# Performance work log

Measured on AMD Instinct MI355X. Metric: run time of the kernel, lower is better.

## Reference

```python
import jax, jax.numpy as jnp
import numpy as np

HEADS = 4
OUT_DIM = 64
NEG_SLOPE = 0.2


def setup_inputs() -> dict:
    key = jax.random.key(0)
    k1, k2, k3, k4 = jax.random.split(key, 4)
    n, in_dim = 4096, 256
    x = jax.random.normal(k1, (n, in_dim), dtype=jnp.float32)
    adj = jax.random.randint(k2, (n, n), 0, 2, dtype=jnp.int32)
    # lin: in_dim -> heads*out_dim (no bias), stored as [in_dim, heads*out_dim]
    W = jax.random.normal(k3, (in_dim, HEADS * OUT_DIM), dtype=jnp.float32) * 0.05
    # att_weight: [heads, 2*out_dim]
    att = jax.random.normal(k4, (HEADS, 2 * OUT_DIM), dtype=jnp.float32) * 0.05
    return {"x": x, "adj": adj, "W": W, "att": att}


def reference(x, adj, W, att):
    n = x.shape[0]
    h = (x @ W).reshape(n, HEADS, OUT_DIM)  # [n, H, D]
    # scores[i,j,h] = att[h] . cat(h_i, h_j) = <h_i, a_src[h]> + <h_j, a_dst[h]>
    a_src, a_dst = att[:, :OUT_DIM], att[:, OUT_DIM:]
    e_src = jnp.einsum('nhd,hd->nh', h, a_src)  # [n, H]
    e_dst = jnp.einsum('nhd,hd->nh', h, a_dst)  # [n, H]
    scores = e_src[:, None, :] + e_dst[None, :, :]  # [n, n, H]
    scores = jax.nn.leaky_relu(scores, negative_slope=NEG_SLOPE)
    mask = (adj > 0)[:, :, None]  # [n, n, 1]
    scores = jnp.where(mask, scores, -jnp.inf)
    alpha = jax.nn.softmax(scores, axis=1)  # softmax over neighbors j
    # h_prime[i,h,d] = sum_j alpha[i,j,h] * h[j,h,d]
    h_prime = jnp.einsum('ijh,jhd->ihd', alpha, h)
    return h_prime.reshape(n, HEADS * OUT_DIM)
```

## Files before the change

kernel.cpp:

```cpp
#include <hip/hip_runtime.h>
#include <hip/hip_bf16.h>

#define HEADS 4
#define ODIM 64
#define HD 256
#define NEG_SLOPE 0.2f
#define SPLITS 8

typedef __attribute__((ext_vector_type(8))) short bf16x8;
typedef __attribute__((ext_vector_type(4))) float floatx4;
typedef __attribute__((ext_vector_type(2))) float floatx2;

__global__ __launch_bounds__(256) void pack_xw(const float* __restrict__ x,
                                               const float* __restrict__ W,
                                               __hip_bfloat16* __restrict__ xh,
                                               __hip_bfloat16* __restrict__ xl,
                                               __hip_bfloat16* __restrict__ wh,
                                               __hip_bfloat16* __restrict__ wl,
                                               int K, int nxb) {
    const int b = blockIdx.x;
    const int Kc = K >> 5;
    if (b < nxb) {
        const int g = b * 256 + threadIdx.x;
        const int lane = g & 63, frag = g >> 6;
        const int kc = frag % Kc, mc = frag / Kc;
        const int l16 = lane & 15, q = lane >> 4;
        const float* src = x + (size_t)(mc * 16 + l16) * K + kc * 32 + q * 8;
        const float4 v0 = *(const float4*)src;
        const float4 v1 = *(const float4*)(src + 4);
        const float vv[8] = {v0.x, v0.y, v0.z, v0.w, v1.x, v1.y, v1.z, v1.w};
        union { __hip_bfloat16 b[8]; bf16x8 v; } H, L;
        #pragma unroll
        for (int p = 0; p < 8; ++p) {
            H.b[p] = __float2bfloat16(vv[p]);
            L.b[p] = __float2bfloat16(vv[p] - __bfloat162float(H.b[p]));
        }
        *(bf16x8*)&xh[(size_t)frag * 512 + lane * 8] = H.v;
        *(bf16x8*)&xl[(size_t)frag * 512 + lane * 8] = L.v;
    } else {
        const int g = (b - nxb) * 256 + threadIdx.x;
        const int lane = g & 63, frag = g >> 6;
        const int kc = frag % Kc, nc = frag / Kc;
        const int l16 = lane & 15, q = lane >> 4;
        union { __hip_bfloat16 b[8]; bf16x8 v; } H, L;
        #pragma unroll
        for (int p = 0; p < 8; ++p) {
            const float w = W[(size_t)(kc * 32 + q * 8 + p) * HD + nc * 16 + l16];
            H.b[p] = __float2bfloat16(w);
            L.b[p] = __float2bfloat16(w - __bfloat162float(H.b[p]));
        }
        *(bf16x8*)&wh[(size_t)frag * 512 + lane * 8] = H.v;
        *(bf16x8*)&wl[(size_t)frag * 512 + lane * 8] = L.v;
    }
}

__global__ __launch_bounds__(128) void gemm_fused(
    const __hip_bfloat16* __restrict__ xh, const __hip_bfloat16* __restrict__ xl,
    const __hip_bfloat16* __restrict__ wh, const __hip_bfloat16* __restrict__ wl,
    const float* __restrict__ att, float2* __restrict__ esrc, float2* __restrict__ edst,
    __hip_bfloat16* __restrict__ hbB, int n, int K) {

    __shared__ __hip_bfloat16 T[64][40];

    const int tid = threadIdx.x, wave = tid >> 6, lane = tid & 63;
    const int q = lane >> 4, l16 = lane & 15;
    const int m0 = blockIdx.x * 32;
    const int head = blockIdx.y;
    const int Kc = K >> 5;
    const int mc = (m0 >> 4) + wave;

    floatx4 acc[4] = {{0.f,0.f,0.f,0.f},{0.f,0.f,0.f,0.f},{0.f,0.f,0.f,0.f},{0.f,0.f,0.f,0.f}};

    const __hip_bfloat16* Axh = xh + (size_t)mc * Kc * 512 + lane * 8;
    const __hip_bfloat16* Axl = xl + (size_t)mc * Kc * 512 + lane * 8;
    const __hip_bfloat16* Bwh = wh + lane * 8;
    const __hip_bfloat16* Bwl = wl + lane * 8;
    #pragma unroll 2
    for (int kc = 0; kc < Kc; ++kc) {
        const bf16x8 ah = *(const bf16x8*)(Axh + (size_t)kc * 512);
        const bf16x8 al = *(const bf16x8*)(Axl + (size_t)kc * 512);
        bf16x8 bh[4], bl[4];
        #pragma unroll
        for (int nt = 0; nt < 4; ++nt) {
            const size_t fo = (size_t)((head * 4 + nt) * Kc + kc) * 512;
            bh[nt] = *(const bf16x8*)(Bwh + fo);
            bl[nt] = *(const bf16x8*)(Bwl + fo);
        }
        #pragma unroll
        for (int nt = 0; nt < 4; ++nt)
            acc[nt] = __builtin_amdgcn_mfma_f32_16x16x32_bf16(ah, bh[nt], acc[nt], 0, 0, 0);
        #pragma unroll
        for (int nt = 0; nt < 4; ++nt)
            acc[nt] = __builtin_amdgcn_mfma_f32_16x16x32_bf16(ah, bl[nt], acc[nt], 0, 0, 0);
        #pragma unroll
        for (int nt = 0; nt < 4; ++nt)
            acc[nt] = __builtin_amdgcn_mfma_f32_16x16x32_bf16(al, bh[nt], acc[nt], 0, 0, 0);
    }

    float as_v[4], ad_v[4];
    #pragma unroll
    for (int nt = 0; nt < 4; ++nt) {
        as_v[nt] = att[head * 2 * ODIM + nt * 16 + l16];
        ad_v[nt] = att[head * 2 * ODIM + ODIM + nt * 16 + l16];
    }
    #pragma unroll
    for (int r = 0; r < 4; ++r) {
        float ps = 0.f, pd = 0.f;
        #pragma unroll
        for (int nt = 0; nt < 4; ++nt) {
            ps = fmaf(acc[nt][r], as_v[nt], ps);
            pd = fmaf(acc[nt][r], ad_v[nt], pd);
        }
        #pragma unroll
        for (int m = 1; m <= 8; m <<= 1) {
            ps += __shfl_xor(ps, m, 64);
            pd += __shfl_xor(pd, m, 64);
        }
        if (l16 == 0) {
            const int i = m0 + wave * 16 + q * 4 + r;
            esrc[head * n + i] = make_float2(__expf(ps), __expf(NEG_SLOPE * ps));
            edst[head * n + i] = make_float2(__expf(pd), __expf(NEG_SLOPE * pd));
        }
    }

    #pragma unroll
    for (int nt = 0; nt < 4; ++nt) {
        union { __hip_bfloat16 b[4]; uint2 u; } pk;
        #pragma unroll
        for (int r = 0; r < 4; ++r) pk.b[r] = __float2bfloat16(acc[nt][r]);
        *(uint2*)&T[nt * 16 + l16][wave * 16 + q * 4] = pk.u;
    }
    __syncthreads();

    #pragma unroll
    for (int ffi = 0; ffi < 2; ++ffi) {
        const int f = wave + ffi * 2;
        const bf16x8 v = *(const bf16x8*)&T[f * 16 + l16][q * 8];
        const size_t frag = ((size_t)head * (n >> 5) + (m0 >> 5)) * 4 + f;
        *(bf16x8*)&hbB[frag * 512 + lane * 8] = v;
    }
}

__global__ __launch_bounds__(256, 3) void aggregate(
    const int* __restrict__ adj, const float2* __restrict__ esrc,
    const float2* __restrict__ edst, const __hip_bfloat16* __restrict__ hbB,
    float* __restrict__ outsp, float* __restrict__ densp, int n, int KR) {

    __shared__ unsigned char bitsL[32][68];
    __shared__ float2 edL[HEADS][512];

    const int tid = threadIdx.x;
    const int wave = tid >> 6, lane = tid & 63;
    const int q = lane >> 4, l16 = lane & 15;
    const int i0 = blockIdx.x * 32;
    const int K0 = blockIdx.y * KR;

    {
        const int r0 = i0 + wave * 8;
        #pragma unroll
        for (int rr = 0; rr < 8; ++rr) {
            const int4* ap = (const int4*)(adj + (size_t)(r0 + rr) * n + K0 + lane * 8);
            const int4 a = ap[0], b = ap[1];
            unsigned int by = (unsigned int)(a.x > 0)
                            | ((unsigned int)(a.y > 0) << 1)
                            | ((unsigned int)(a.z > 0) << 2)
                            | ((unsigned int)(a.w > 0) << 3)
                            | ((unsigned int)(b.x > 0) << 4)
                            | ((unsigned int)(b.y > 0) << 5)
                            | ((unsigned int)(b.z > 0) << 6)
                            | ((unsigned int)(b.w > 0) << 7);
            bitsL[wave * 8 + rr][lane] = (unsigned char)by;
        }
    }
    for (int t = tid; t < HEADS * 512; t += 256) {
        const int h = t >> 9, j = t & 511;
        edL[h][j] = edst[(size_t)h * n + K0 + j];
    }

    floatx2 es12[2];
    #pragma unroll
    for (int mt = 0; mt < 2; ++mt) {
        const float2 e = esrc[wave * n + i0 + mt * 16 + l16];
        es12[mt][0] = e.x; es12[mt][1] = e.y;
    }

    union { short s[8]; bf16x8 v; } bones;
    #pragma unroll
    for (int p = 0; p < 8; ++p) bones.s[p] = (l16 == 0) ? (short)0x3F80 : (short)0;

    floatx4 acc[2][4];
    floatx4 accd[2];
    #pragma unroll
    for (int mt = 0; mt < 2; ++mt) {
        accd[mt] = (floatx4){0.f, 0.f, 0.f, 0.f};
        #pragma unroll
        for (int nt = 0; nt < 4; ++nt) acc[mt][nt] = (floatx4){0.f, 0.f, 0.f, 0.f};
    }

    __syncthreads();

    const __hip_bfloat16* hb = hbB + ((size_t)wave * (n >> 5) + (K0 >> 5)) * 4 * 512 + lane * 8;
    const int NSTEP = KR >> 5;

    auto loadBF = [&](int s, bf16x8* dst) {
        #pragma unroll
        for (int nt = 0; nt < 4; ++nt)
            dst[nt] = *(const bf16x8*)&hb[((size_t)s * 4 + nt) * 512];
    };

    auto computeStep = [&](int s, const bf16x8* bfr) {
        const unsigned int bm0 = (*(const unsigned int*)&bitsL[l16][s * 4] >> (q * 8)) & 0xFFu;
        const unsigned int bm1 = (*(const unsigned int*)&bitsL[16 + l16][s * 4] >> (q * 8)) & 0xFFu;
        const float4* ep = (const float4*)&edL[wave][s * 32 + q * 8];
        const float4 e01 = ep[0], e23 = ep[1], e45 = ep[2], e67 = ep[3];
        floatx2 ed[8];
        ed[0][0]=e01.x; ed[0][1]=e01.y;  ed[1][0]=e01.z; ed[1][1]=e01.w;
        ed[2][0]=e23.x; ed[2][1]=e23.y;  ed[3][0]=e23.z; ed[3][1]=e23.w;
        ed[4][0]=e45.x; ed[4][1]=e45.y;  ed[5][0]=e45.z; ed[5][1]=e45.w;
        ed[6][0]=e67.x; ed[6][1]=e67.y;  ed[7][0]=e67.z; ed[7][1]=e67.w;
        #pragma unroll
        for (int mt = 0; mt < 2; ++mt) {
            const unsigned int bm = mt ? bm1 : bm0;
            union { unsigned int u[4]; bf16x8 v; } af;
            #pragma unroll
            for (int p = 0; p < 4; ++p) {
                const floatx2 pa = es12[mt] * ed[2 * p];
                const floatx2 pb = es12[mt] * ed[2 * p + 1];
                const float wa = fmaxf(pa[0], pa[1]);
                const float wb = fmaxf(pb[0], pb[1]);
                const unsigned int mm = ((bm >> (2 * p)) & 1u) * 0xFFFFu
                                      | ((bm >> (2 * p + 1)) & 1u) * 0xFFFF0000u;
                af.u[p] = __builtin_amdgcn_perm(__float_as_uint(wb), __float_as_uint(wa),
                                                0x07060302u) & mm;
            }
            #pragma unroll
            for (int nt = 0; nt < 4; ++nt)
                acc[mt][nt] = __builtin_amdgcn_mfma_f32_16x16x32_bf16(af.v, bfr[nt], acc[mt][nt], 0, 0, 0);
            accd[mt] = __builtin_amdgcn_mfma_f32_16x16x32_bf16(af.v, bones.v, accd[mt], 0, 0, 0);
        }
    };

    bf16x8 bA[4], bB[4];
    loadBF(0, bA);
    loadBF(1, bB);
    for (int s = 0; s < NSTEP; s += 2) {
        computeStep(s, bA);
        if (s + 2 < NSTEP) loadBF(s + 2, bA);
        computeStep(s + 1, bB);
        if (s + 3 < NSTEP) loadBF(s + 3, bB);
    }

    const size_t sOut = (size_t)blockIdx.y * n * HD;
    #pragma unroll
    for (int mt = 0; mt < 2; ++mt)
        #pragma unroll
        for (int nt = 0; nt < 4; ++nt)
            #pragma unroll
            for (int r = 0; r < 4; ++r)
                outsp[sOut + (size_t)(i0 + mt * 16 + q * 4 + r) * HD + wave * ODIM + nt * 16 + l16] = acc[mt][nt][r];
    if (l16 == 0) {
        #pragma unroll
        for (int mt = 0; mt < 2; ++mt)
            #pragma unroll
            for (int r = 0; r < 4; ++r)
                densp[((size_t)blockIdx.y * n + i0 + mt * 16 + q * 4 + r) * HEADS + wave] = accd[mt][r];
    }
}

__global__ __launch_bounds__(256) void normalize(const float* __restrict__ outsp,
                                                 const float* __restrict__ densp,
                                                 float* __restrict__ out, int n, int splits) {
    const int g = blockIdx.x * 256 + threadIdx.x;
    const int i = g >> 6;
    const int c4 = (g & 63) * 4;
    const int head = c4 >> 6;
    float den = 0.f;
    for (int s = 0; s < splits; ++s) den += densp[((size_t)s * n + i) * HEADS + head];
    float4 v = {0.f, 0.f, 0.f, 0.f};
    for (int s = 0; s < splits; ++s) {
        const float4 t = *(const float4*)&outsp[(size_t)s * n * HD + (size_t)i * HD + c4];
        v.x += t.x; v.y += t.y; v.z += t.z; v.w += t.w;
    }
    const float inv = 1.0f / den;
    v.x *= inv; v.y *= inv; v.z *= inv; v.w *= inv;
    *(float4*)&out[(size_t)i * HD + c4] = v;
}

extern "C" void kernel_launch(void* const* d_in, const int* in_sizes, int n_in,
                              void* d_out, int out_size, void* d_ws, size_t ws_size,
                              hipStream_t stream) {
    const float* x   = (const float*)d_in[0];
    const int*   adj = (const int*)d_in[1];
    const float* W   = (const float*)d_in[2];
    const float* att = (const float*)d_in[3];
    float* out = (float*)d_out;

    const int in_dim = in_sizes[2] / HD;
    const int n = in_sizes[0] / in_dim;

    char* ws = (char*)d_ws;
    size_t off = 0;
    auto alloc = [&](size_t bytes) -> void* {
        void* p = ws + off; off += (bytes + 255) & ~(size_t)255; return p;
    };
    __hip_bfloat16* xh = (__hip_bfloat16*)alloc((size_t)n * in_dim * 2);
    __hip_bfloat16* xl = (__hip_bfloat16*)alloc((size_t)n * in_dim * 2);
    __hip_bfloat16* wh = (__hip_bfloat16*)alloc((size_t)in_dim * HD * 2);
    __hip_bfloat16* wl = (__hip_bfloat16*)alloc((size_t)in_dim * HD * 2);
    float2* esrc = (float2*)alloc((size_t)HEADS * n * 8);
    float2* edst = (float2*)alloc((size_t)HEADS * n * 8);
    __hip_bfloat16* hbB = (__hip_bfloat16*)alloc((size_t)n * HD * 2);

    const size_t outB = (size_t)n * HD * 4, denB = (size_t)n * HEADS * 4;
    float* densp = (float*)alloc((size_t)SPLITS * denB);
    float* outsp = (float*)alloc((size_t)SPLITS * outB);

    const int nxb = (n / 16) * (in_dim / 32) * 64 / 256;
    const int nwb = (HD / 16) * (in_dim / 32) * 64 / 256;
    pack_xw<<<nxb + nwb, 256, 0, stream>>>(x, W, xh, xl, wh, wl, in_dim, nxb);
    gemm_fused<<<dim3(n / 32, HEADS), 128, 0, stream>>>(xh, xl, wh, wl, att, esrc, edst, hbB, n, in_dim);
    aggregate<<<dim3(n / 32, SPLITS), 256, 0, stream>>>(adj, esrc, edst, hbB, outsp, densp, n, n / SPLITS);
    normalize<<<n * 64 / 256, 256, 0, stream>>>(outsp, densp, out, n, SPLITS);
}
```

Measured before the change: 144.0 us.

## Precompress adjacency to bitmask and restructure aggregate per-head with LDS-staged features

Adds a separate kernel that packs the int32 adjacency matrix into a bitmask using wave ballots. The aggregate kernel now reads that bitmask. Each block handles 256 rows for a single head, and the per-head feature fragments are staged through double-buffered shared memory so the four waves share them. The goal is to cut how often each block rereads adjacency and feature data from global memory, at the cost of an extra kernel launch, more registers per thread (occupancy hint lowered from 3 to 2), and per-chunk barriers.

```diff
diff --git a/kernel.cpp b/kernel.cpp
--- a/kernel.cpp
+++ b/kernel.cpp
@@ -6,6 +6,7 @@
 #define HD 256
 #define NEG_SLOPE 0.2f
 #define SPLITS 8
+#define MI 256
 
 typedef __attribute__((ext_vector_type(8))) short bf16x8;
 typedef __attribute__((ext_vector_type(4))) float floatx4;
@@ -54,6 +55,26 @@
     }
 }
 
+__global__ __launch_bounds__(256) void compress_adj(const int* __restrict__ adj,
+                                                    unsigned int* __restrict__ bits, int n) {
+    const int wave = threadIdx.x >> 6, lane = threadIdx.x & 63;
+    const int i = blockIdx.y;
+    const int j0 = blockIdx.x * 1024 + wave * 256;
+    unsigned long long m[4];
+    #pragma unroll
+    for (int k = 0; k < 4; ++k)
+        m[k] = __ballot(adj[(size_t)i * n + j0 + k * 64 + lane] > 0);
+    if (lane == 0) {
+        uint4 u, v;
+        u.x = (unsigned)m[0]; u.y = (unsigned)(m[0] >> 32);
+        u.z = (unsigned)m[1]; u.w = (unsigned)(m[1] >> 32);
+        v.x = (unsigned)m[2]; v.y = (unsigned)(m[2] >> 32);
+        v.z = (unsigned)m[3]; v.w = (unsigned)(m[3] >> 32);
+        *(uint4*)&bits[(size_t)i * (n >> 5) + (j0 >> 5)] = u;
+        *(uint4*)&bits[(size_t)i * (n >> 5) + (j0 >> 5) + 4] = v;
+    }
+}
+
 __global__ __launch_bounds__(128) void gemm_fused(
     const __hip_bfloat16* __restrict__ xh, const __hip_bfloat16* __restrict__ xl,
     const __hip_bfloat16* __restrict__ wh, const __hip_bfloat16* __restrict__ wl,
@@ -141,46 +162,38 @@
     }
 }
 
-__global__ __launch_bounds__(256, 3) void aggregate(
-    const int* __restrict__ adj, const float2* __restrict__ esrc,
+__global__ __launch_bounds__(256, 2) void aggregate(
+    const unsigned int* __restrict__ bits, const float2* __restrict__ esrc,
     const float2* __restrict__ edst, const __hip_bfloat16* __restrict__ hbB,
     float* __restrict__ outsp, float* __restrict__ densp, int n, int KR) {
 
-    __shared__ unsigned char bitsL[32][68];
-    __shared__ float2 edL[HEADS][512];
+    __shared__ unsigned int bitsL[MI][17];
+    __shared__ float2 edL[512];
+    __shared__ __hip_bfloat16 hbL[2][8][512];
 
     const int tid = threadIdx.x;
     const int wave = tid >> 6, lane = tid & 63;
     const int q = lane >> 4, l16 = lane & 15;
-    const int i0 = blockIdx.x * 32;
-    const int K0 = blockIdx.y * KR;
+    const int i0 = blockIdx.x * MI;
+    const int head = blockIdx.y;
+    const int K0 = blockIdx.z * KR;
+    const int nw = n >> 5;
 
     {
-        const int r0 = i0 + wave * 8;
-        #pragma unroll
-        for (int rr = 0; rr < 8; ++rr) {
-            const int4* ap = (const int4*)(adj + (size_t)(r0 + rr) * n + K0 + lane * 8);
-            const int4 a = ap[0], b = ap[1];
-            unsigned int by = (unsigned int)(a.x > 0)
-                            | ((unsigned int)(a.y > 0) << 1)
-                            | ((unsigned int)(a.z > 0) << 2)
-                            | ((unsigned int)(a.w > 0) << 3)
-                            | ((unsigned int)(b.x > 0) << 4)
-                            | ((unsigned int)(b.y > 0) << 5)
-                            | ((unsigned int)(b.z > 0) << 6)
-                            | ((unsigned int)(b.w > 0) << 7);
-            bitsL[wave * 8 + rr][lane] = (unsigned char)by;
-        }
-    }
-    for (int t = tid; t < HEADS * 512; t += 256) {
-        const int h = t >> 9, j = t & 511;
-        edL[h][j] = edst[(size_t)h * n + K0 + j];
-    }
-
-    floatx2 es12[2];
-    #pragma unroll
-    for (int mt = 0; mt < 2; ++mt) {
-        const float2 e = esrc[wave * n + i0 + mt * 16 + l16];
+        const int dw = tid & 15, rb = tid >> 4;
+        #pragma unroll
+        for (int rr = 0; rr < 16; ++rr) {
+            const int row = rr * 16 + rb;
+            bitsL[row][dw] = bits[(size_t)(i0 + row) * nw + (K0 >> 5) + dw];
+        }
+    }
+    for (int t = tid; t < KR; t += 256)
+        edL[t] = edst[(size_t)head * n + K0 + t];
+
+    floatx2 es12[4];
+    #pragma unroll
+    for (int mt = 0; mt < 4; ++mt) {
+        const float2 e = esrc[head * n + i0 + wave * 64 + mt * 16 + l16];
         es12[mt][0] = e.x; es12[mt][1] = e.y;
     }
 
@@ -188,39 +201,47 @@
     #pragma unroll
     for (int p = 0; p < 8; ++p) bones.s[p] = (l16 == 0) ? (short)0x3F80 : (short)0;
 
-    floatx4 acc[2][4];
-    floatx4 accd[2];
-    #pragma unroll
-    for (int mt = 0; mt < 2; ++mt) {
+    floatx4 acc[4][4];
+    floatx4 accd[4];
+    #pragma unroll
+    for (int mt = 0; mt < 4; ++mt) {
         accd[mt] = (floatx4){0.f, 0.f, 0.f, 0.f};
         #pragma unroll
         for (int nt = 0; nt < 4; ++nt) acc[mt][nt] = (floatx4){0.f, 0.f, 0.f, 0.f};
     }
 
-    __syncthreads();
-
-    const __hip_bfloat16* hb = hbB + ((size_t)wave * (n >> 5) + (K0 >> 5)) * 4 * 512 + lane * 8;
-    const int NSTEP = KR >> 5;
-
-    auto loadBF = [&](int s, bf16x8* dst) {
-        #pragma unroll
-        for (int nt = 0; nt < 4; ++nt)
-            dst[nt] = *(const bf16x8*)&hb[((size_t)s * 4 + nt) * 512];
+    const __hip_bfloat16* hbsrc = hbB + ((size_t)head * (n >> 5) + (K0 >> 5)) * 4 * 512;
+
+    uint4 stg0, stg1;
+    auto loadChunk = [&](int c) {
+        const uint4* src = (const uint4*)(hbsrc + (size_t)c * 4096);
+        stg0 = src[tid * 2];
+        stg1 = src[tid * 2 + 1];
     };
-
-    auto computeStep = [&](int s, const bf16x8* bfr) {
-        const unsigned int bm0 = (*(const unsigned int*)&bitsL[l16][s * 4] >> (q * 8)) & 0xFFu;
-        const unsigned int bm1 = (*(const unsigned int*)&bitsL[16 + l16][s * 4] >> (q * 8)) & 0xFFu;
-        const float4* ep = (const float4*)&edL[wave][s * 32 + q * 8];
+    auto writeChunk = [&](int buf) {
+        uint4* dst = (uint4*)&hbL[buf][0][0];
+        dst[tid * 2] = stg0;
+        dst[tid * 2 + 1] = stg1;
+    };
+
+    auto computeStep = [&](int buf, int sIn, int s) {
+        unsigned int bm[4];
+        #pragma unroll
+        for (int mt = 0; mt < 4; ++mt)
+            bm[mt] = (bitsL[wave * 64 + mt * 16 + l16][s] >> (q * 8)) & 0xFFu;
+        const float4* ep = (const float4*)&edL[s * 32 + q * 8];
         const float4 e01 = ep[0], e23 = ep[1], e45 = ep[2], e67 = ep[3];
         floatx2 ed[8];
         ed[0][0]=e01.x; ed[0][1]=e01.y;  ed[1][0]=e01.z; ed[1][1]=e01.w;
         ed[2][0]=e23.x; ed[2][1]=e23.y;  ed[3][0]=e23.z; ed[3][1]=e23.w;
         ed[4][0]=e45.x; ed[4][1]=e45.y;  ed[5][0]=e45.z; ed[5][1]=e45.w;
         ed[6][0]=e67.x; ed[6][1]=e67.y;  ed[7][0]=e67.z; ed[7][1]=e67.w;
-        #pragma unroll
-        for (int mt = 0; mt < 2; ++mt) {
-            const unsigned int bm = mt ? bm1 : bm0;
+        bf16x8 bfr[4];
+        #pragma unroll
+        for (int nt = 0; nt < 4; ++nt)
+            bfr[nt] = *(const bf16x8*)&hbL[buf][sIn * 4 + nt][lane * 8];
+        #pragma unroll
+        for (int mt = 0; mt < 4; ++mt) {
             union { unsigned int u[4]; bf16x8 v; } af;
             #pragma unroll
             for (int p = 0; p < 4; ++p) {
@@ -228,8 +249,8 @@
                 const floatx2 pb = es12[mt] * ed[2 * p + 1];
                 const float wa = fmaxf(pa[0], pa[1]);
                 const float wb = fmaxf(pb[0], pb[1]);
-                const unsigned int mm = ((bm >> (2 * p)) & 1u) * 0xFFFFu
-                                      | ((bm >> (2 * p + 1)) & 1u) * 0xFFFF0000u;
+                const unsigned int mm = ((bm[mt] >> (2 * p)) & 1u) * 0xFFFFu
+                                      | ((bm[mt] >> (2 * p + 1)) & 1u) * 0xFFFF0000u;
                 af.u[p] = __builtin_amdgcn_perm(__float_as_uint(wb), __float_as_uint(wa),
                                                 0x07060302u) & mm;
             }
@@ -240,30 +261,39 @@
         }
     };
 
-    bf16x8 bA[4], bB[4];
-    loadBF(0, bA);
-    loadBF(1, bB);
-    for (int s = 0; s < NSTEP; s += 2) {
-        computeStep(s, bA);
-        if (s + 2 < NSTEP) loadBF(s + 2, bA);
-        computeStep(s + 1, bB);
-        if (s + 3 < NSTEP) loadBF(s + 3, bB);
-    }
-
-    const size_t sOut = (size_t)blockIdx.y * n * HD;
-    #pragma unroll
-    for (int mt = 0; mt < 2; ++mt)
+    loadChunk(0);
+    writeChunk(0);
+    __syncthreads();
+
+    const int NCH = KR >> 6;
+    int cur = 0;
+    for (int c = 0; c < NCH; ++c) {
+        if (c + 1 < NCH) loadChunk(c + 1);
+        computeStep(cur, 0, c * 2);
+        computeStep(cur, 1, c * 2 + 1);
+        if (c + 1 < NCH) {
+            writeChunk(cur ^ 1);
+            __syncthreads();
+            cur ^= 1;
+        }
+    }
+
+    const size_t sOut = (size_t)blockIdx.z * n * HD;
+    #pragma unroll
+    for (int mt = 0; mt < 4; ++mt)
         #pragma unroll
         for (int nt = 0; nt < 4; ++nt)
             #pragma unroll
             for (int r = 0; r < 4; ++r)
-                outsp[sOut + (size_t)(i0 + mt * 16 + q * 4 + r) * HD + wave * ODIM + nt * 16 + l16] = acc[mt][nt][r];
+                outsp[sOut + (size_t)(i0 + wave * 64 + mt * 16 + q * 4 + r) * HD
+                      + head * ODIM + nt * 16 + l16] = acc[mt][nt][r];
     if (l16 == 0) {
         #pragma unroll
-        for (int mt = 0; mt < 2; ++mt)
+        for (int mt = 0; mt < 4; ++mt)
             #pragma unroll
             for (int r = 0; r < 4; ++r)
-                densp[((size_t)blockIdx.y * n + i0 + mt * 16 + q * 4 + r) * HEADS + wave] = accd[mt][r];
+                densp[((size_t)blockIdx.z * n + i0 + wave * 64 + mt * 16 + q * 4 + r) * HEADS + head]
+                    = accd[mt][r];
     }
 }
 
@@ -310,6 +340,7 @@
     float2* esrc = (float2*)alloc((size_t)HEADS * n * 8);
     float2* edst = (float2*)alloc((size_t)HEADS * n * 8);
     __hip_bfloat16* hbB = (__hip_bfloat16*)alloc((size_t)n * HD * 2);
+    unsigned int* bits = (unsigned int*)alloc((size_t)n * (n / 8));
 
     const size_t outB = (size_t)n * HD * 4, denB = (size_t)n * HEADS * 4;
     float* densp = (float*)alloc((size_t)SPLITS * denB);
@@ -318,7 +349,8 @@
     const int nxb = (n / 16) * (in_dim / 32) * 64 / 256;
     const int nwb = (HD / 16) * (in_dim / 32) * 64 / 256;
     pack_xw<<<nxb + nwb, 256, 0, stream>>>(x, W, xh, xl, wh, wl, in_dim, nxb);
+    compress_adj<<<dim3(n / 1024, n), 256, 0, stream>>>(adj, bits, n);
     gemm_fused<<<dim3(n / 32, HEADS), 128, 0, stream>>>(xh, xl, wh, wl, att, esrc, edst, hbB, n, in_dim);
-    aggregate<<<dim3(n / 32, SPLITS), 256, 0, stream>>>(adj, esrc, edst, hbB, outsp, densp, n, n / SPLITS);
+    aggregate<<<dim3(n / MI, HEADS, SPLITS), 256, 0, stream>>>(bits, esrc, edst, hbB, outsp, densp, n, n / SPLITS);
     normalize<<<n * 64 / 256, 256, 0, stream>>>(outsp, densp, out, n, SPLITS);
 }
```

New measurement: 147.9 us. 1.03x slower.
